# Kernel tuning notes

Measured on AMD Instinct MI355X. Metric: run time of the kernel, lower is better.

The kernel has to match this reference:

```python
import jax, jax.numpy as jnp
import numpy as np

N_NODES = 50000
N_EDGES = 800000
IN_F = 128
HID = 64
HEADS = 4
N_CLASSES = 256
NEG_SLOPE = 0.2


def _gat_layer(h, W, al, ar, b, src, dst, act):
    """One DGL-style GATConv. h:[N,Din], W:[Din,H*F], al/ar:[H,F], b:[H*F].
    Returns [N,H,F]."""
    N = h.shape[0]
    H, F = al.shape
    z = (h @ W).reshape(N, H, F)                       # projected feats
    el = jnp.einsum('nhf,hf->nh', z, al)               # [N,H] src score part
    er = jnp.einsum('nhf,hf->nh', z, ar)               # [N,H] dst score part
    e = jax.nn.leaky_relu(el[src] + er[dst], negative_slope=NEG_SLOPE)  # [E,H]
    # segment softmax over incoming edges of each destination node
    emax = jax.ops.segment_max(e, dst, num_segments=N)                  # [N,H]
    ex = jnp.exp(e - emax[dst])                                         # [E,H]
    den = jax.ops.segment_sum(ex, dst, num_segments=N)                  # [N,H]
    alpha = ex / jnp.maximum(den[dst], 1e-9)                            # [E,H]
    msg = z[src] * alpha[:, :, None]                                    # [E,H,F]
    out = jax.ops.segment_sum(msg, dst, num_segments=N)                 # [N,H,F]
    out = out + b.reshape(1, H, F)
    return act(out) if act is not None else out


def setup_inputs() -> dict:
    key = jax.random.key(0)
    ks = jax.random.split(key, 16)
    feat = jax.random.normal(ks[0], (N_NODES, IN_F), dtype=jnp.float32)
    src = jax.random.randint(ks[1], (N_EDGES,), 0, N_NODES, dtype=jnp.int32)
    dst = jax.random.randint(ks[2], (N_EDGES,), 0, N_NODES, dtype=jnp.int32)

    def glorot(k, shape):
        fan = shape[0] + shape[-1]
        return jax.random.normal(k, shape, dtype=jnp.float32) * np.sqrt(2.0 / fan)

    # layer 0: IN_F -> HEADS*HID
    W0 = glorot(ks[3], (IN_F, HEADS * HID))
    al0 = glorot(ks[4], (HEADS, HID))
    ar0 = glorot(ks[5], (HEADS, HID))
    b0 = jnp.zeros((HEADS * HID,), dtype=jnp.float32)
    # layer 1: HEADS*HID -> HEADS*HID
    W1 = glorot(ks[6], (HEADS * HID, HEADS * HID))
    al1 = glorot(ks[7], (HEADS, HID))
    ar1 = glorot(ks[8], (HEADS, HID))
    b1 = jnp.zeros((HEADS * HID,), dtype=jnp.float32)
    # final layer: HEADS*HID -> HEADS*N_CLASSES
    W2 = glorot(ks[9], (HEADS * HID, HEADS * N_CLASSES))
    al2 = glorot(ks[10], (HEADS, N_CLASSES))
    ar2 = glorot(ks[11], (HEADS, N_CLASSES))
    b2 = jnp.zeros((HEADS * N_CLASSES,), dtype=jnp.float32)
    return {"feat": feat,
            "W0": W0, "al0": al0, "ar0": ar0, "b0": b0,
            "W1": W1, "al1": al1, "ar1": ar1, "b1": b1,
            "W2": W2, "al2": al2, "ar2": ar2, "b2": b2,
            "src": src, "dst": dst}


def reference(feat, W0, al0, ar0, b0, W1, al1, ar1, b1, W2, al2, ar2, b2, src, dst):
    elu = jax.nn.elu
    h = _gat_layer(feat, W0, al0, ar0, b0, src, dst, elu).reshape(N_NODES, -1)
    h = _gat_layer(h, W1, al1, ar1, b1, src, dst, elu).reshape(N_NODES, -1)
    logits = _gat_layer(h, W2, al2, ar2, b2, src, dst, None).mean(axis=1)  # [N, C]
    return logits
```

## Files before the change

### kernel.cpp

```cpp
#include <hip/hip_runtime.h>
#include <hip/hip_bf16.h>


#define NN 50000
#define NE 800000
#define NH_HEADS 4

typedef __attribute__((ext_vector_type(8))) short short8;
typedef __attribute__((ext_vector_type(8))) _Float16 half8;
typedef __attribute__((ext_vector_type(4))) _Float16 half4;
typedef __attribute__((ext_vector_type(4))) float floatx4;

__device__ inline float bf2f(short s) {
    union { unsigned u; float f; } v; v.u = ((unsigned)(unsigned short)s) << 16;
    return v.f;
}
__device__ inline short f2bf_rne(float x) {
    union { float f; unsigned u; } v; v.f = x;
    unsigned r = v.u + 0x7fff + ((v.u >> 16) & 1);
    return (short)(r >> 16);
}
__device__ inline void split1(float x, short& h, short& l) {
    union { float f; unsigned u; } v; v.f = x;
    h = (short)(v.u >> 16);
    union { float f; unsigned u; } rv; rv.f = v.f - bf2f(h);
    l = (short)(rv.u >> 16);
}


__global__ void hist_kernel(const int* __restrict__ dst, int* __restrict__ deg, int E) {
    int e = blockIdx.x * 256 + threadIdx.x;
    if (e < E) atomicAdd(&deg[dst[e]], 1);
}

__global__ void scan_block_kernel(const int* __restrict__ deg, int* __restrict__ offs,
                                  int* __restrict__ bsums, int n) {
    __shared__ int s[256];
    int tid = threadIdx.x;
    int i = blockIdx.x * 256 + tid;
    int v = (i < n) ? deg[i] : 0;
    s[tid] = v;
    __syncthreads();
    for (int off = 1; off < 256; off <<= 1) {
        int x = (tid >= off) ? s[tid - off] : 0;
        __syncthreads();
        s[tid] += x;
        __syncthreads();
    }
    if (i < n) offs[i] = s[tid] - v;
    if (tid == 255) bsums[blockIdx.x] = s[255];
}

__global__ void scan_sums_kernel(const int* __restrict__ bsums, int* __restrict__ boffs, int nb) {
    __shared__ int s[256];
    int tid = threadIdx.x;
    int v = (tid < nb) ? bsums[tid] : 0;
    s[tid] = v;
    __syncthreads();
    for (int off = 1; off < 256; off <<= 1) {
        int x = (tid >= off) ? s[tid - off] : 0;
        __syncthreads();
        s[tid] += x;
        __syncthreads();
    }
    boffs[tid] = s[tid] - v;
}

__global__ void add_offs_kernel(int* __restrict__ offs, const int* __restrict__ boffs,
                                int* __restrict__ cursor, int n, int total) {
    int i = blockIdx.x * 256 + threadIdx.x;
    if (i < n) {
        int o = offs[i] + boffs[blockIdx.x];
        offs[i] = o;
        cursor[i] = o;
    }
    if (i == 0) offs[n] = total;
}

__global__ void scatter_kernel(const int* __restrict__ src, const int* __restrict__ dst,
                               int* __restrict__ cursor, int* __restrict__ psrc, int E) {
    int e = blockIdx.x * 256 + threadIdx.x;
    if (e < E) {
        int p = atomicAdd(&cursor[dst[e]], 1);
        psrc[p] = src[e];
    }
}


__global__ __launch_bounds__(256) void splitA_perm(const float* __restrict__ A,
                                                   short* __restrict__ hi,
                                                   short* __restrict__ lo,
                                                   int total) {
    int tid = blockIdx.x * 256 + threadIdx.x;
    if (tid >= total) return;
    int n = tid >> 4, o = tid & 15;
    const float* p = A + (size_t)n * 128 + o * 8;
    float4 x0 = ((const float4*)p)[0];
    float4 x1 = ((const float4*)p)[1];
    float xs[8] = {x0.x, x0.y, x0.z, x0.w, x1.x, x1.y, x1.z, x1.w};
    short8 hv, lv;
#pragma unroll
    for (int j = 0; j < 8; ++j) { short h, l; split1(xs[j], h, l); hv[j] = h; lv[j] = l; }
    size_t idx = ((size_t)(n >> 4) * 4 + (o >> 2)) * 64 + (n & 15) + 16 * (o & 3);
    ((short8*)hi)[idx] = hv;
    ((short8*)lo)[idx] = lv;
}


__global__ __launch_bounds__(256) void splitB_kernel(const float* __restrict__ B,
                                                     short* __restrict__ hi,
                                                     short* __restrict__ lo,
                                                     int K, int N) {
    int tid = blockIdx.x * 256 + threadIdx.x;
    int NG = N >> 4;
    int total = (K >> 5) * NG * 64;
    if (tid >= total) return;
    int lane = tid & 63;
    int rc = tid >> 6;
    int g = rc % NG, c = rc / NG;
    int n = g * 16 + (lane & 15);
    int k = c * 32 + (lane >> 4) * 8;
    short8 hv, lv;
#pragma unroll
    for (int j = 0; j < 8; ++j) {
        float x = B[(size_t)(k + j) * N + n];
        short h = f2bf_rne(x);
        hv[j] = h;
        lv[j] = f2bf_rne(x - bf2f(h));
    }
    ((short8*)hi)[tid] = hv;
    ((short8*)lo)[tid] = lv;
}

__global__ __launch_bounds__(256) void splitB_f16_kernel(const float* __restrict__ B,
                                                         _Float16* __restrict__ hi,
                                                         _Float16* __restrict__ lo,
                                                         int K, int N) {
    int tid = blockIdx.x * 256 + threadIdx.x;
    int NG = N >> 4;
    int total = (K >> 5) * NG * 64;
    if (tid >= total) return;
    int lane = tid & 63;
    int rc = tid >> 6;
    int g = rc % NG, c = rc / NG;
    int n = g * 16 + (lane & 15);
    int k = c * 32 + (lane >> 4) * 8;
    half8 hv, lv;
#pragma unroll
    for (int j = 0; j < 8; ++j) {
        float x = B[(size_t)(k + j) * N + n];
        _Float16 h = (_Float16)x;
        hv[j] = h;
        lv[j] = (_Float16)(x - (float)h);
    }
    ((half8*)hi)[tid] = hv;
    ((half8*)lo)[tid] = lv;
}

__global__ __launch_bounds__(256) void splitB2_f16s_kernel(const float* __restrict__ W2,
                                                           _Float16* __restrict__ hi) {
    int tid = blockIdx.x * 256 + threadIdx.x;
    const int NG = 16;
    int total = (1024 >> 5) * NG * 64;
    if (tid >= total) return;
    int lane = tid & 63;
    int rc = tid >> 6;
    int g = rc % NG, c = rc / NG;
    int n = g * 16 + (lane & 15);
    int kk = c * 32 + (lane >> 4) * 8;
    half8 hv;
#pragma unroll
    for (int j = 0; j < 8; ++j) {
        int kg = kk + j;
        int h = kg >> 8, k = kg & 255;
        hv[j] = (_Float16)W2[(size_t)k * 1024 + h * 256 + n];
    }
    ((half8*)hi)[tid] = hv;
}


__device__ inline floatx4 mfma16(short8 a, short8 b, floatx4 c) {
    return __builtin_amdgcn_mfma_f32_16x16x32_bf16(a, b, c, 0, 0, 0);
}
__device__ inline floatx4 mfma16h(half8 a, half8 b, floatx4 c) {
    return __builtin_amdgcn_mfma_f32_16x16x32_f16(a, b, c, 0, 0, 0);
}

__global__ __launch_bounds__(256) void gemm_n256l(const short* __restrict__ Ahi,
                                                  const short* __restrict__ Alo,
                                                  const short* __restrict__ Bh,
                                                  const short* __restrict__ Bl,
                                                  _Float16* __restrict__ Cf,
                                                  const float* __restrict__ alv,
                                                  const float* __restrict__ arv,
                                                  float* __restrict__ elo,
                                                  float* __restrict__ ero,
                                                  int M, int K) {
    int KC = K >> 5;
    int t = threadIdx.x;
    int lane = t & 63;
    int w = t >> 6;
    int bm = blockIdx.x * 64;
    int tile0 = blockIdx.x * 4;
    int g0 = w * 4;
    const short8* pAh = (const short8*)Ahi;
    const short8* pAl = (const short8*)Alo;
    const short8* pBh = (const short8*)Bh;
    const short8* pBl = (const short8*)Bl;

    floatx4 acc[4][4] = {};

    for (int c = 0; c < KC; ++c) {
        short8 ah[4], al4[4], bh[4], bl[4];
#pragma unroll
        for (int mt = 0; mt < 4; ++mt) {
            size_t ia = ((size_t)(tile0 + mt) * KC + c) * 64 + lane;
            ah[mt] = pAh[ia];
            al4[mt] = pAl[ia];
        }
#pragma unroll
        for (int g = 0; g < 4; ++g) {
            size_t ib = ((size_t)c * 16 + g0 + g) * 64 + lane;
            bh[g] = pBh[ib];
            bl[g] = pBl[ib];
        }
#pragma unroll
        for (int mt = 0; mt < 4; ++mt) {
#pragma unroll
            for (int g = 0; g < 4; ++g) {
                acc[mt][g] = mfma16(ah[mt], bh[g], acc[mt][g]);
                acc[mt][g] = mfma16(al4[mt], bh[g], acc[mt][g]);
                acc[mt][g] = mfma16(ah[mt], bl[g], acc[mt][g]);
            }
        }
    }

    int rowb = bm + (lane >> 4) * 4;
    int colb = w * 64 + (lane & 15);
#pragma unroll
    for (int mt = 0; mt < 4; ++mt) {
#pragma unroll
        for (int r = 0; r < 4; ++r) {
            int rr = rowb + mt * 16 + r;
            if (rr < M) {
#pragma unroll
                for (int g = 0; g < 4; ++g) {
                    Cf[(size_t)rr * 256 + colb + g * 16] = (_Float16)acc[mt][g][r];
                }
            }
        }
    }

    if (alv) {
        float alr[4], arr_[4];
#pragma unroll
        for (int g = 0; g < 4; ++g) {
            int f = w * 64 + (lane & 15) + g * 16;
            alr[g] = alv[f];
            arr_[g] = arv[f];
        }
#pragma unroll
        for (int mt = 0; mt < 4; ++mt) {
#pragma unroll
            for (int r = 0; r < 4; ++r) {
                float se = acc[mt][0][r] * alr[0] + acc[mt][1][r] * alr[1] +
                           acc[mt][2][r] * alr[2] + acc[mt][3][r] * alr[3];
                float sr = acc[mt][0][r] * arr_[0] + acc[mt][1][r] * arr_[1] +
                           acc[mt][2][r] * arr_[2] + acc[mt][3][r] * arr_[3];
                se += __shfl_xor(se, 1); se += __shfl_xor(se, 2);
                se += __shfl_xor(se, 4); se += __shfl_xor(se, 8);
                sr += __shfl_xor(sr, 1); sr += __shfl_xor(sr, 2);
                sr += __shfl_xor(sr, 4); sr += __shfl_xor(sr, 8);
                int rr = rowb + mt * 16 + r;
                if ((lane & 15) == 0 && rr < M) {
                    elo[rr * 4 + w] = se;
                    ero[rr * 4 + w] = sr;
                }
            }
        }
    }
}

__global__ __launch_bounds__(256) void gemm_f16_n256(const _Float16* __restrict__ A,
                                                     const _Float16* __restrict__ Bh,
                                                     const _Float16* __restrict__ Bl,
                                                     const float* __restrict__ bias4,
                                                     float* __restrict__ C,
                                                     _Float16* __restrict__ Cf,
                                                     const float* __restrict__ alv,
                                                     const float* __restrict__ arv,
                                                     float* __restrict__ elo,
                                                     float* __restrict__ ero,
                                                     int M, int K) {
    int KC = K >> 5;
    int t = threadIdx.x;
    int lane = t & 63;
    int w = t >> 6;
    int bm = blockIdx.x * 64;
    int tile0 = blockIdx.x * 4;
    int g0 = w * 4;
    const half8* pA = (const half8*)A;
    const half8* pBh = (const half8*)Bh;
    const half8* pBl = (const half8*)Bl;
    bool dual = (Bl != nullptr);

    floatx4 acc[4][4] = {};

    for (int c = 0; c < KC; ++c) {
        half8 a[4], bh[4], bl[4];
#pragma unroll
        for (int mt = 0; mt < 4; ++mt) {
            a[mt] = pA[((size_t)(tile0 + mt) * KC + c) * 64 + lane];
        }
#pragma unroll
        for (int g = 0; g < 4; ++g) {
            bh[g] = pBh[((size_t)c * 16 + g0 + g) * 64 + lane];
        }
        if (dual) {
#pragma unroll
            for (int g = 0; g < 4; ++g) {
                bl[g] = pBl[((size_t)c * 16 + g0 + g) * 64 + lane];
            }
        }
#pragma unroll
        for (int mt = 0; mt < 4; ++mt) {
#pragma unroll
            for (int g = 0; g < 4; ++g) {
                acc[mt][g] = mfma16h(a[mt], bh[g], acc[mt][g]);
            }
            if (dual) {
#pragma unroll
                for (int g = 0; g < 4; ++g) {
                    acc[mt][g] = mfma16h(a[mt], bl[g], acc[mt][g]);
                }
            }
        }
    }

    int rowb = bm + (lane >> 4) * 4;
    int colb = w * 64 + (lane & 15);
#pragma unroll
    for (int mt = 0; mt < 4; ++mt) {
#pragma unroll
        for (int r = 0; r < 4; ++r) {
            int rr = rowb + mt * 16 + r;
            if (rr < M) {
#pragma unroll
                for (int g = 0; g < 4; ++g) {
                    int col = colb + g * 16;
                    float v = acc[mt][g][r];
                    if (bias4) {
                        v = 0.25f * (v + bias4[col] + bias4[col + 256] +
                                     bias4[col + 512] + bias4[col + 768]);
                    }
                    if (Cf) Cf[(size_t)rr * 256 + col] = (_Float16)v;
                    else    C[(size_t)rr * 256 + col] = v;
                }
            }
        }
    }

    if (alv) {
        float alr[4], arr_[4];
#pragma unroll
        for (int g = 0; g < 4; ++g) {
            int f = w * 64 + (lane & 15) + g * 16;
            alr[g] = alv[f];
            arr_[g] = arv[f];
        }
#pragma unroll
        for (int mt = 0; mt < 4; ++mt) {
#pragma unroll
            for (int r = 0; r < 4; ++r) {
                float se = acc[mt][0][r] * alr[0] + acc[mt][1][r] * alr[1] +
                           acc[mt][2][r] * alr[2] + acc[mt][3][r] * alr[3];
                float sr = acc[mt][0][r] * arr_[0] + acc[mt][1][r] * arr_[1] +
                           acc[mt][2][r] * arr_[2] + acc[mt][3][r] * arr_[3];
                se += __shfl_xor(se, 1); se += __shfl_xor(se, 2);
                se += __shfl_xor(se, 4); se += __shfl_xor(se, 8);
                sr += __shfl_xor(sr, 1); sr += __shfl_xor(sr, 2);
                sr += __shfl_xor(sr, 4); sr += __shfl_xor(sr, 8);
                int rr = rowb + mt * 16 + r;
                if ((lane & 15) == 0 && rr < M) {
                    elo[rr * 4 + w] = se;
                    ero[rr * 4 + w] = sr;
                }
            }
        }
    }
}


__global__ __launch_bounds__(256) void proj_av_kernel(const float* __restrict__ W2,
                                                      const float* __restrict__ al2,
                                                      const float* __restrict__ ar2,
                                                      float* __restrict__ val,
                                                      float* __restrict__ var_) {
    int gid = blockIdx.x * 256 + threadIdx.x;
    int w = gid >> 6;
    int lane = threadIdx.x & 63;
    if (w >= 1024) return;
    int h = w >> 8, k = w & 255;
    const float* wrow = W2 + (size_t)k * 1024 + h * 256;
    const float* ap = al2 + h * 256;
    const float* rp = ar2 + h * 256;
    float sv = 0.f, sr = 0.f;
    for (int j = lane; j < 256; j += 64) {
        float x = wrow[j];
        sv += x * ap[j];
        sr += x * rp[j];
    }
#pragma unroll
    for (int off = 32; off > 0; off >>= 1) {
        sv += __shfl_down(sv, off);
        sr += __shfl_down(sr, off);
    }
    if (lane == 0) { val[w] = sv; var_[w] = sr; }
}

__global__ __launch_bounds__(256) void elr2_kernel(const _Float16* __restrict__ h1,
                                                   const float* __restrict__ val,
                                                   const float* __restrict__ var_,
                                                   float* __restrict__ el,
                                                   float* __restrict__ er) {
    int gid = blockIdx.x * 256 + threadIdx.x;
    int w = gid >> 6;
    int lane = threadIdx.x & 63;
    if (w >= NN * 4) return;
    int n = w >> 2, h = w & 3;
    const _Float16* hr = h1 + (size_t)n * 256;
    const float* vp = val + h * 256;
    const float* rp = var_ + h * 256;
    float se = 0.f, sr = 0.f;
    for (int k = lane; k < 256; k += 64) {
        float x = (float)hr[k];
        se += x * vp[k];
        sr += x * rp[k];
    }
#pragma unroll
    for (int off = 32; off > 0; off >>= 1) {
        se += __shfl_down(se, off);
        sr += __shfl_down(sr, off);
    }
    if (lane == 0) { el[w] = se; er[w] = sr; }
}


__global__ __launch_bounds__(64) void agg_z64_kernel(const _Float16* __restrict__ z,
                                                     const float* __restrict__ el,
                                                     const float* __restrict__ er,
                                                     const int* __restrict__ offs,
                                                     const int* __restrict__ psrc,
                                                     const float* __restrict__ bias,
                                                     _Float16* __restrict__ out,
                                                     int perm) {
    int n = blockIdx.x;
    int l = threadIdx.x;
    __shared__ float p_lds[16][4];
    __shared__ int src_lds[16];
    __shared__ float den_lds[4];
    if (l < 4) den_lds[l] = 0.f;
    int e_local = l >> 2, hh = l & 3;
    int h = l >> 4;
    float er_n = er[n * 4 + hh];
    int beg = offs[n], end = offs[n + 1];
    float a0 = 0.f, a1 = 0.f, a2 = 0.f, a3 = 0.f;
    for (int base = beg; base < end; base += 16) {
        int cnt = min(16, end - base);
        __syncthreads();
        float p = 0.f;
        if (e_local < cnt) {
            int s = psrc[base + e_local];
            if (hh == 0) src_lds[e_local] = s;
            float sc = el[s * 4 + hh] + er_n;
            sc = (sc > 0.f) ? sc : 0.2f * sc;
            p = __expf(sc);
            p_lds[e_local][hh] = p;
        }
        float d = p;
        d += __shfl_xor(d, 4);  d += __shfl_xor(d, 8);
        d += __shfl_xor(d, 16); d += __shfl_xor(d, 32);
        if (l < 4) den_lds[l] += d;
        __syncthreads();
        for (int e = 0; e < cnt; ++e) {
            half4 v = *(const half4*)(z + (size_t)src_lds[e] * 256 + (l << 2));
            float pe = p_lds[e][h];
            a0 += pe * (float)v[0];
            a1 += pe * (float)v[1];
            a2 += pe * (float)v[2];
            a3 += pe * (float)v[3];
        }
    }
    __syncthreads();
    float rd = 1.f / fmaxf(den_lds[h], 1e-9f);
    float vals[4] = {a0, a1, a2, a3};
    half4 o;
#pragma unroll
    for (int j = 0; j < 4; ++j) {
        float x = vals[j] * rd + bias[(l << 2) + j];
        x = (x > 0.f) ? x : (__expf(x) - 1.f);
        o[j] = (_Float16)x;
    }
    if (perm) {
        size_t off = ((((size_t)(n >> 4) * 8 + (l >> 3)) * 64 +
                       (n & 15) + 16 * ((l >> 1) & 3)) << 3) + ((l & 1) << 2);
        *(half4*)(out + off) = o;
    } else {
        *(half4*)(out + (size_t)n * 256 + (l << 2)) = o;
    }
}

__global__ __launch_bounds__(64) void aggH_64_kernel(const _Float16* __restrict__ h1,
                                                     const float* __restrict__ el,
                                                     const float* __restrict__ er,
                                                     const int* __restrict__ offs,
                                                     const int* __restrict__ psrc,
                                                     _Float16* __restrict__ oA) {
    int n = blockIdx.x;
    int l = threadIdx.x;
    __shared__ __align__(16) float p_lds[16][4];
    __shared__ int src_lds[16];
    __shared__ float den_lds[4];
    if (l < 4) den_lds[l] = 0.f;
    int e_local = l >> 2, hh = l & 3;
    float er_n = er[n * 4 + hh];
    int beg = offs[n], end = offs[n + 1];
    float acc[4][4] = {};
    for (int base = beg; base < end; base += 16) {
        int cnt = min(16, end - base);
        __syncthreads();
        float p = 0.f;
        if (e_local < cnt) {
            int s = psrc[base + e_local];
            if (hh == 0) src_lds[e_local] = s;
            float sc = el[s * 4 + hh] + er_n;
            sc = (sc > 0.f) ? sc : 0.2f * sc;
            p = __expf(sc);
            p_lds[e_local][hh] = p;
        }
        float d = p;
        d += __shfl_xor(d, 4);  d += __shfl_xor(d, 8);
        d += __shfl_xor(d, 16); d += __shfl_xor(d, 32);
        if (l < 4) den_lds[l] += d;
        __syncthreads();
        for (int e = 0; e < cnt; ++e) {
            half4 v = *(const half4*)(h1 + (size_t)src_lds[e] * 256 + (l << 2));
            float vf0 = (float)v[0], vf1 = (float)v[1];
            float vf2 = (float)v[2], vf3 = (float)v[3];
            floatx4 pv = *(const floatx4*)&p_lds[e][0];
#pragma unroll
            for (int hd = 0; hd < 4; ++hd) {
                acc[hd][0] += pv[hd] * vf0;
                acc[hd][1] += pv[hd] * vf1;
                acc[hd][2] += pv[hd] * vf2;
                acc[hd][3] += pv[hd] * vf3;
            }
        }
    }
    __syncthreads();
    size_t tb = (size_t)(n >> 4) * 32;
    int lane_in = (n & 15) + 16 * ((l >> 1) & 3);
    int j0 = (l & 1) << 2;
#pragma unroll
    for (int hd = 0; hd < 4; ++hd) {
        float rd = 1.f / fmaxf(den_lds[hd], 1e-9f);
        half4 o;
#pragma unroll
        for (int j = 0; j < 4; ++j) o[j] = (_Float16)(acc[hd][j] * rd);
        size_t off = (((tb + hd * 8 + (l >> 3)) * 64 + lane_in) << 3) + j0;
        *(half4*)(oA + off) = o;
    }
}


extern "C" void kernel_launch(void* const* d_in, const int* in_sizes, int n_in,
                              void* d_out, int out_size, void* d_ws, size_t ws_size,
                              hipStream_t stream) {
    const float* feat = (const float*)d_in[0];
    const float* W0 = (const float*)d_in[1];
    const float* al0 = (const float*)d_in[2];
    const float* ar0 = (const float*)d_in[3];
    const float* b0 = (const float*)d_in[4];
    const float* W1 = (const float*)d_in[5];
    const float* al1 = (const float*)d_in[6];
    const float* ar1 = (const float*)d_in[7];
    const float* b1 = (const float*)d_in[8];
    const float* W2 = (const float*)d_in[9];
    const float* al2 = (const float*)d_in[10];
    const float* ar2 = (const float*)d_in[11];
    const float* b2 = (const float*)d_in[12];
    const int* src = (const int*)d_in[13];
    const int* dst = (const int*)d_in[14];
    float* out = (float*)d_out;

    int mb64 = (NN + 63) / 64;
    size_t TIL = (size_t)mb64 * 4;

    float* slotA = (float*)d_ws;
    _Float16* zh = (_Float16*)slotA;
    short* feathi = (short*)(slotA + (size_t)NN * 256);
    short* featlo = feathi + TIL * 4 * 512;
    _Float16* Af16 = (_Float16*)slotA;
    float* slotB = slotA + (size_t)NN * 1024;
    _Float16* h0f = (_Float16*)slotB;
    _Float16* h1h = (_Float16*)slotB;
    float* el = slotB + (size_t)NN * 256;
    float* er = el + (size_t)NN * NH_HEADS;
    int* deg = (int*)(er + (size_t)NN * NH_HEADS);
    int* offs = deg + NN;
    int* cursor = offs + NN + 2;
    int* bsums = cursor + NN;
    int* boffs = bsums + 256;
    int* psrc = boffs + 256;
    short* Bh = (short*)(psrc + NE + 2);
    short* Bl = Bh + 262144;
    float* val = (float*)(Bl + 262144);
    float* var_ = val + 1024;

    hipMemsetAsync(deg, 0, NN * sizeof(int), stream);
    hist_kernel<<<(NE + 255) / 256, 256, 0, stream>>>(dst, deg, NE);
    int nb = (NN + 255) / 256;
    scan_block_kernel<<<nb, 256, 0, stream>>>(deg, offs, bsums, NN);
    scan_sums_kernel<<<1, 256, 0, stream>>>(bsums, boffs, nb);
    add_offs_kernel<<<nb, 256, 0, stream>>>(offs, boffs, cursor, NN, NE);
    scatter_kernel<<<(NE + 255) / 256, 256, 0, stream>>>(src, dst, cursor, psrc, NE);

    splitA_perm<<<(NN * 16 + 255) / 256, 256, 0, stream>>>(feat, feathi, featlo, NN * 16);
    splitB_kernel<<<(4096 + 255) / 256, 256, 0, stream>>>(W0, Bh, Bl, 128, 256);
    gemm_n256l<<<mb64, 256, 0, stream>>>(feathi, featlo, Bh, Bl, zh,
                                         al0, ar0, el, er, NN, 128);
    agg_z64_kernel<<<NN, 64, 0, stream>>>(zh, el, er, offs, psrc, b0, h0f, 1);

    splitB_f16_kernel<<<(8192 + 255) / 256, 256, 0, stream>>>(W1, (_Float16*)Bh,
                                                              (_Float16*)Bl, 256, 256);
    gemm_f16_n256<<<mb64, 256, 0, stream>>>(h0f, (const _Float16*)Bh, (const _Float16*)Bl,
                                            nullptr, nullptr, zh, al1, ar1, el, er,
                                            NN, 256);
    agg_z64_kernel<<<NN, 64, 0, stream>>>(zh, el, er, offs, psrc, b1, h1h, 0);

    proj_av_kernel<<<256, 256, 0, stream>>>(W2, al2, ar2, val, var_);
    elr2_kernel<<<NN, 256, 0, stream>>>(h1h, val, var_, el, er);
    aggH_64_kernel<<<NN, 64, 0, stream>>>(h1h, el, er, offs, psrc, Af16);
    splitB2_f16s_kernel<<<(32768 + 255) / 256, 256, 0, stream>>>(W2, (_Float16*)Bh);
    gemm_f16_n256<<<mb64, 256, 0, stream>>>(Af16, (const _Float16*)Bh, nullptr,
                                            b2, out, nullptr, nullptr, nullptr,
                                            nullptr, nullptr, NN, 1024);
}
```

Before: 668.6 us.

## Switch GEMM A operands from MFMA-permuted tiles to plain row-major layout

```diff
diff --git a/kernel.cpp b/kernel.cpp
--- a/kernel.cpp
+++ b/kernel.cpp
@@ -87,23 +87,21 @@
 }
 
 
-__global__ __launch_bounds__(256) void splitA_perm(const float* __restrict__ A,
-                                                   short* __restrict__ hi,
-                                                   short* __restrict__ lo,
-                                                   int total) {
+__global__ __launch_bounds__(256) void splitA_rm(const float* __restrict__ A,
+                                                 short* __restrict__ hi,
+                                                 short* __restrict__ lo,
+                                                 int total8) {
     int tid = blockIdx.x * 256 + threadIdx.x;
-    if (tid >= total) return;
-    int n = tid >> 4, o = tid & 15;
-    const float* p = A + (size_t)n * 128 + o * 8;
+    if (tid >= total8) return;
+    const float* p = A + (size_t)tid * 8;
     float4 x0 = ((const float4*)p)[0];
     float4 x1 = ((const float4*)p)[1];
     float xs[8] = {x0.x, x0.y, x0.z, x0.w, x1.x, x1.y, x1.z, x1.w};
     short8 hv, lv;
 #pragma unroll
     for (int j = 0; j < 8; ++j) { short h, l; split1(xs[j], h, l); hv[j] = h; lv[j] = l; }
-    size_t idx = ((size_t)(n >> 4) * 4 + (o >> 2)) * 64 + (n & 15) + 16 * (o & 3);
-    ((short8*)hi)[idx] = hv;
-    ((short8*)lo)[idx] = lv;
+    ((short8*)hi)[tid] = hv;
+    ((short8*)lo)[tid] = lv;
 }
 
 
@@ -201,22 +199,28 @@
     int lane = t & 63;
     int w = t >> 6;
     int bm = blockIdx.x * 64;
-    int tile0 = blockIdx.x * 4;
     int g0 = w * 4;
-    const short8* pAh = (const short8*)Ahi;
-    const short8* pAl = (const short8*)Alo;
     const short8* pBh = (const short8*)Bh;
     const short8* pBl = (const short8*)Bl;
 
+    const short* pAh_[4];
+    const short* pAl_[4];
+#pragma unroll
+    for (int mt = 0; mt < 4; ++mt) {
+        int r = bm + mt * 16 + (lane & 15);
+        if (r >= M) r = M - 1;
+        pAh_[mt] = Ahi + (size_t)r * K + ((lane >> 4) << 3);
+        pAl_[mt] = Alo + (size_t)r * K + ((lane >> 4) << 3);
+    }
+
     floatx4 acc[4][4] = {};
 
     for (int c = 0; c < KC; ++c) {
         short8 ah[4], al4[4], bh[4], bl[4];
 #pragma unroll
         for (int mt = 0; mt < 4; ++mt) {
-            size_t ia = ((size_t)(tile0 + mt) * KC + c) * 64 + lane;
-            ah[mt] = pAh[ia];
-            al4[mt] = pAl[ia];
+            ah[mt] = *(const short8*)(pAh_[mt] + c * 32);
+            al4[mt] = *(const short8*)(pAl_[mt] + c * 32);
         }
 #pragma unroll
         for (int g = 0; g < 4; ++g) {
@@ -297,20 +301,26 @@
     int lane = t & 63;
     int w = t >> 6;
     int bm = blockIdx.x * 64;
-    int tile0 = blockIdx.x * 4;
     int g0 = w * 4;
-    const half8* pA = (const half8*)A;
     const half8* pBh = (const half8*)Bh;
     const half8* pBl = (const half8*)Bl;
     bool dual = (Bl != nullptr);
 
+    const _Float16* pA_[4];
+#pragma unroll
+    for (int mt = 0; mt < 4; ++mt) {
+        int r = bm + mt * 16 + (lane & 15);
+        if (r >= M) r = M - 1;
+        pA_[mt] = A + (size_t)r * K + ((lane >> 4) << 3);
+    }
+
     floatx4 acc[4][4] = {};
 
     for (int c = 0; c < KC; ++c) {
         half8 a[4], bh[4], bl[4];
 #pragma unroll
         for (int mt = 0; mt < 4; ++mt) {
-            a[mt] = pA[((size_t)(tile0 + mt) * KC + c) * 64 + lane];
+            a[mt] = *(const half8*)(pA_[mt] + c * 32);
         }
 #pragma unroll
         for (int g = 0; g < 4; ++g) {
@@ -452,8 +462,7 @@
                                                      const int* __restrict__ offs,
                                                      const int* __restrict__ psrc,
                                                      const float* __restrict__ bias,
-                                                     _Float16* __restrict__ out,
-                                                     int perm) {
+                                                     _Float16* __restrict__ out) {
     int n = blockIdx.x;
     int l = threadIdx.x;
     __shared__ float p_lds[16][4];
@@ -501,13 +510,7 @@
         x = (x > 0.f) ? x : (__expf(x) - 1.f);
         o[j] = (_Float16)x;
     }
-    if (perm) {
-        size_t off = ((((size_t)(n >> 4) * 8 + (l >> 3)) * 64 +
-                       (n & 15) + 16 * ((l >> 1) & 3)) << 3) + ((l & 1) << 2);
-        *(half4*)(out + off) = o;
-    } else {
-        *(half4*)(out + (size_t)n * 256 + (l << 2)) = o;
-    }
+    *(half4*)(out + (size_t)n * 256 + (l << 2)) = o;
 }
 
 __global__ __launch_bounds__(64) void aggH_64_kernel(const _Float16* __restrict__ h1,
@@ -558,17 +561,14 @@
         }
     }
     __syncthreads();
-    size_t tb = (size_t)(n >> 4) * 32;
-    int lane_in = (n & 15) + 16 * ((l >> 1) & 3);
-    int j0 = (l & 1) << 2;
+    size_t base_o = (size_t)n * 1024 + (l << 2);
 #pragma unroll
     for (int hd = 0; hd < 4; ++hd) {
         float rd = 1.f / fmaxf(den_lds[hd], 1e-9f);
         half4 o;
 #pragma unroll
         for (int j = 0; j < 4; ++j) o[j] = (_Float16)(acc[hd][j] * rd);
-        size_t off = (((tb + hd * 8 + (l >> 3)) * 64 + lane_in) << 3) + j0;
-        *(half4*)(oA + off) = o;
+        *(half4*)(oA + base_o + hd * 256) = o;
     }
 }
 
@@ -593,13 +593,10 @@
     const int* dst = (const int*)d_in[14];
     float* out = (float*)d_out;
 
-    int mb64 = (NN + 63) / 64;
-    size_t TIL = (size_t)mb64 * 4;
-
     float* slotA = (float*)d_ws;
     _Float16* zh = (_Float16*)slotA;
     short* feathi = (short*)(slotA + (size_t)NN * 256);
-    short* featlo = feathi + TIL * 4 * 512;
+    short* featlo = feathi + (size_t)NN * 128;
     _Float16* Af16 = (_Float16*)slotA;
     float* slotB = slotA + (size_t)NN * 1024;
     _Float16* h0f = (_Float16*)slotB;
@@ -625,18 +622,20 @@
     add_offs_kernel<<<nb, 256, 0, stream>>>(offs, boffs, cursor, NN, NE);
     scatter_kernel<<<(NE + 255) / 256, 256, 0, stream>>>(src, dst, cursor, psrc, NE);
 
-    splitA_perm<<<(NN * 16 + 255) / 256, 256, 0, stream>>>(feat, feathi, featlo, NN * 16);
+    int mb64 = (NN + 63) / 64;
+
+    splitA_rm<<<(NN * 128 / 8 + 255) / 256, 256, 0, stream>>>(feat, feathi, featlo, NN * 128 / 8);
     splitB_kernel<<<(4096 + 255) / 256, 256, 0, stream>>>(W0, Bh, Bl, 128, 256);
     gemm_n256l<<<mb64, 256, 0, stream>>>(feathi, featlo, Bh, Bl, zh,
                                          al0, ar0, el, er, NN, 128);
-    agg_z64_kernel<<<NN, 64, 0, stream>>>(zh, el, er, offs, psrc, b0, h0f, 1);
+    agg_z64_kernel<<<NN, 64, 0, stream>>>(zh, el, er, offs, psrc, b0, h0f);
 
     splitB_f16_kernel<<<(8192 + 255) / 256, 256, 0, stream>>>(W1, (_Float16*)Bh,
                                                               (_Float16*)Bl, 256, 256);
     gemm_f16_n256<<<mb64, 256, 0, stream>>>(h0f, (const _Float16*)Bh, (const _Float16*)Bl,
                                             nullptr, nullptr, zh, al1, ar1, el, er,
                                             NN, 256);
-    agg_z64_kernel<<<NN, 64, 0, stream>>>(zh, el, er, offs, psrc, b1, h1h, 0);
+    agg_z64_kernel<<<NN, 64, 0, stream>>>(zh, el, er, offs, psrc, b1, h1h);
 
     proj_av_kernel<<<256, 256, 0, stream>>>(W2, al2, ar2, val, var_);
     elr2_kernel<<<NN, 256, 0, stream>>>(h1h, val, var_, el, er);
```

New measurement: 618.5 us. -7.5%, faster.
